# Kernel tuning notes

Measured on AMD Instinct MI355X. Metric: run time of the kernel, lower is better.

## Reference

```python
import jax, jax.numpy as jnp
import numpy as np

B, T, C, H = 4, 2048, 1024, 16
HS = C // H  # head_size = 64


def setup_inputs() -> dict:
    key = jax.random.key(0)
    ks = jax.random.split(key, 6)
    s = C ** -0.5  # Linear default init scale (approx, kaiming-uniform-ish)
    x = jax.random.normal(ks[0], (B, T, C), dtype=jnp.float32)
    Wq = jax.random.normal(ks[1], (H, C, HS), dtype=jnp.float32) * s
    Wk = jax.random.normal(ks[2], (H, C, HS), dtype=jnp.float32) * s
    Wv = jax.random.normal(ks[3], (H, C, HS), dtype=jnp.float32) * s
    Wproj = jax.random.normal(ks[4], (C, C), dtype=jnp.float32) * s
    bproj = jax.random.normal(ks[5], (C,), dtype=jnp.float32) * s
    return {"x": x, "Wq": Wq, "Wk": Wk, "Wv": Wv, "Wproj": Wproj, "bproj": bproj}


def reference(x, Wq, Wk, Wv, Wproj, bproj):
    # Batched multi-head attention equivalent to looping over per-head modules.
    # q,k,v: (B, H, T, HS)
    q = jnp.einsum('btc,hcd->bhtd', x, Wq)
    k = jnp.einsum('btc,hcd->bhtd', x, Wk)
    v = jnp.einsum('btc,hcd->bhtd', x, Wv)
    scale = HS ** -0.5
    scores = jnp.einsum('bhqd,bhkd->bhqk', q, k) * scale  # (B,H,T,T)
    causal = jnp.tril(jnp.ones((T, T), dtype=bool))
    scores = jnp.where(causal, scores, -jnp.inf)
    wei = jax.nn.softmax(scores, axis=-1)
    out_heads = jnp.einsum('bhqk,bhkd->bhqd', wei, v)  # (B,H,T,HS)
    # concat heads along last dim -> (B,T,H*HS) = (B,T,C)
    combo = out_heads.transpose(0, 2, 1, 3).reshape(B, T, C)
    out = jnp.einsum('btc,cd->btd', combo, Wproj.T.T @ jnp.eye(C, dtype=combo.dtype)) if False else combo @ Wproj.T + bproj
    # dropout p=0.0 (eval) -> identity
    return out
```

## Files before the change

kernel.cpp:

```cpp
#include <hip/hip_runtime.h>
#include <stdint.h>

#define B_  4
#define T_  2048
#define C_  1024
#define H_  16
#define HS_ 64
#define M_  (B_*T_)
#define K_  C_

typedef unsigned short u16;
typedef float v4f __attribute__((ext_vector_type(4)));
typedef short v8s __attribute__((ext_vector_type(8)));
typedef u16   v4u __attribute__((ext_vector_type(4)));
typedef unsigned int u32;
typedef u32 v2u32 __attribute__((ext_vector_type(2)));

__device__ __forceinline__ u16 f2bf(float f){
  unsigned u = __float_as_uint(f);
  u += 0x7fffu + ((u >> 16) & 1u);
  return (u16)(u >> 16);
}

__device__ __forceinline__ u32 cvt_pk_bf16(float a, float b){
  u32 r;
  asm("v_cvt_pk_bf16_f32 %0, %1, %2" : "=v"(r) : "v"(a), "v"(b));
  return r;
}

__device__ __forceinline__ void async16(const void* g, void* l){
  __builtin_amdgcn_global_load_lds(
      (const __attribute__((address_space(1))) unsigned int*)g,
      (__attribute__((address_space(3))) unsigned int*)l,
      16, 0, 0);
}


__global__ __launch_bounds__(256)
void prep(const float* __restrict__ x,
          const float* __restrict__ Wq, const float* __restrict__ Wk,
          const float* __restrict__ Wv, const float* __restrict__ Wproj,
          u16* __restrict__ xhat, u16* __restrict__ wallT, u16* __restrict__ wprojT)
{
  const int bid = blockIdx.x;
  if (bid < 4096){
    int gid = bid * 256 + threadIdx.x;
    int r  = gid >> 7;
    int kg = gid & 127;
    const float* s = x + ((size_t)r << 10) + (kg << 3);
    v4f a = *(const v4f*)s;
    v4f b = *(const v4f*)(s + 4);
    union { v8s v; u16 e[8]; } o;
    o.e[0]=f2bf(a[0]); o.e[1]=f2bf(a[1]); o.e[2]=f2bf(a[2]); o.e[3]=f2bf(a[3]);
    o.e[4]=f2bf(b[0]); o.e[5]=f2bf(b[1]); o.e[6]=f2bf(b[2]); o.e[7]=f2bf(b[3]);
    *(v8s*)(xhat + (((size_t)(r >> 4) * 128 + kg) * 128 + ((r & 15) << 3))) = o.v;
  } else if (bid < 5632){
    int gid = (bid - 4096) * 256 + threadIdx.x;
    int n  = gid >> 7;
    int cg = gid & 127;
    int tensor = n >> 10;
    int h = (n >> 6) & 15;
    int d = n & 63;
    const float* W = (tensor == 0) ? Wq : ((tensor == 1) ? Wk : Wv);
    const float* base = W + ((size_t)(h * C_ + cg * 8)) * HS_ + d;
    union { v8s v; u16 e[8]; } o;
    #pragma unroll
    for (int j = 0; j < 8; j++) o.e[j] = f2bf(base[(size_t)j * HS_]);
    *(v8s*)(wallT + (((size_t)(n >> 4) * 128 + cg) * 128 + ((n & 15) << 3))) = o.v;
  } else {
    int gid = (bid - 5632) * 256 + threadIdx.x;
    int r  = gid >> 7;
    int kg = gid & 127;
    const float* s = Wproj + ((size_t)r << 10) + (kg << 3);
    v4f a = *(const v4f*)s;
    v4f b = *(const v4f*)(s + 4);
    union { v8s v; u16 e[8]; } o;
    o.e[0]=f2bf(a[0]); o.e[1]=f2bf(a[1]); o.e[2]=f2bf(a[2]); o.e[3]=f2bf(a[3]);
    o.e[4]=f2bf(b[0]); o.e[5]=f2bf(b[1]); o.e[6]=f2bf(b[2]); o.e[7]=f2bf(b[3]);
    *(v8s*)(wprojT + (((size_t)(r >> 4) * 128 + kg) * 128 + ((r & 15) << 3))) = o.v;
  }
}

#define QSCALE 0.1803368801111204f

template<int MODE>
__global__ __launch_bounds__(256)
void gemm_bt(const u16* __restrict__ A, const u16* __restrict__ Bt,
             const float* __restrict__ bias,
             u16* __restrict__ o0, u16* __restrict__ o1, u16* __restrict__ o2,
             float* __restrict__ o0f)
{
  __shared__ __align__(16) u16 sA[2][128 * 32];
  __shared__ __align__(16) u16 sB[2][128 * 32];
  const int tid  = threadIdx.x;
  const int lane = tid & 63;
  const int wave = tid >> 6;
  const int l15  = lane & 15, quad = lane >> 4;
  const int wm   = wave >> 1, wn = wave & 1;
  const int m0   = blockIdx.y * 128;
  const int n0   = blockIdx.x * 128;
  const int mg0  = blockIdx.y * 8;
  const int ng0  = blockIdx.x * 8;

  v4f acc[4][4] = {};

  const int s0 = tid, s1 = tid + 256;
  const int t0 = s0 >> 6, r0 = s0 & 15, g0 = (s0 >> 4) & 3;
  const int t1 = s1 >> 6, r1 = s1 & 15, g1 = (s1 >> 4) & 3;

  const char* aS0 = (const char*)A  + ((size_t)(mg0 + t0) * 16384 + g0 * 128 + r0 * 8) * 2;
  const char* aS1 = (const char*)A  + ((size_t)(mg0 + t1) * 16384 + g1 * 128 + r1 * 8) * 2;
  const char* bS0 = (const char*)Bt + ((size_t)(ng0 + t0) * 16384 + g0 * 128 + r0 * 8) * 2;
  const char* bS1 = (const char*)Bt + ((size_t)(ng0 + t1) * 16384 + g1 * 128 + r1 * 8) * 2;

  async16(aS0, (char*)sA[0] + s0 * 16);
  async16(aS1, (char*)sA[0] + s1 * 16);
  async16(bS0, (char*)sB[0] + s0 * 16);
  async16(bS1, (char*)sB[0] + s1 * 16);
  __syncthreads();

  int cur = 0;
  for (int kk = 0; kk < K_; kk += 32){
    const int nxt = cur ^ 1;
    if (kk + 32 < K_){
      const size_t off = (size_t)(kk + 32) * 32;
      async16(aS0 + off, (char*)sA[nxt] + s0 * 16);
      async16(aS1 + off, (char*)sA[nxt] + s1 * 16);
      async16(bS0 + off, (char*)sB[nxt] + s0 * 16);
      async16(bS1 + off, (char*)sB[nxt] + s1 * 16);
    }

    v8s af[4], bfr[4];
    const u16* pa = sA[cur] + (size_t)(wm * 4) * 512 + lane * 8;
    const u16* pb = sB[cur] + (size_t)(wn * 4) * 512 + lane * 8;
    #pragma unroll
    for (int mi = 0; mi < 4; mi++) af[mi]  = *(const v8s*)(pa + mi * 512);
    #pragma unroll
    for (int ni = 0; ni < 4; ni++) bfr[ni] = *(const v8s*)(pb + ni * 512);

    #pragma unroll
    for (int mi = 0; mi < 4; mi++)
      #pragma unroll
      for (int ni = 0; ni < 4; ni++)
        acc[mi][ni] = __builtin_amdgcn_mfma_f32_16x16x32_bf16(af[mi], bfr[ni], acc[mi][ni], 0, 0, 0);

    __syncthreads();
    cur = nxt;
  }

  if constexpr (MODE == 0){
    #pragma unroll
    for (int ni = 0; ni < 4; ni++){
      const int ng = n0 + wn * 64 + ni * 16 + l15;
      const int tensor = ng >> 10;
      const int hh = (ng >> 6) & 15;
      const int d  = ng & 63;
      #pragma unroll
      for (int mi = 0; mi < 4; mi++){
        const int mbase = m0 + wm * 64 + mi * 16 + quad * 4;
        const int bb = mbase >> 11;
        const int tt = mbase & 2047;
        if (tensor == 2){
          v4u pk;
          #pragma unroll
          for (int r = 0; r < 4; r++) pk[r] = f2bf(acc[mi][ni][r]);
          *(v4u*)(o2 + ((size_t)((bb * H_ + hh) * HS_ + d)) * T_ + tt) = pk;
        } else if (tensor == 0){
          #pragma unroll
          for (int r = 0; r < 4; r++)
            o0[((size_t)((bb * H_ + hh)) * T_ + tt + r) * HS_ + d] = f2bf(acc[mi][ni][r] * QSCALE);
        } else {
          #pragma unroll
          for (int r = 0; r < 4; r++)
            o1[((size_t)((bb * H_ + hh)) * T_ + tt + r) * HS_ + d] = f2bf(acc[mi][ni][r]);
        }
      }
    }
  } else {
    #pragma unroll
    for (int ni = 0; ni < 4; ni++){
      const int ng = n0 + wn * 64 + ni * 16 + l15;
      const float bv = bias[ng];
      #pragma unroll
      for (int mi = 0; mi < 4; mi++){
        const int mbase = m0 + wm * 64 + mi * 16 + quad * 4;
        #pragma unroll
        for (int r = 0; r < 4; r++)
          o0f[(size_t)(mbase + r) * C_ + ng] = acc[mi][ni][r] + bv;
      }
    }
  }
}

__global__ __launch_bounds__(512, 4)
void attn(const u16* __restrict__ Q, const u16* __restrict__ Kb_, const u16* __restrict__ Vt,
          u16* __restrict__ O)
{
  __shared__ __align__(16) u16 sK[64 * 64];
  __shared__ __align__(16) u16 sV[64 * 64];
  const int tid  = threadIdx.x;
  const int lane = tid & 63;
  const int wave = tid >> 6;
  const int l15  = lane & 15, quad = lane >> 4;
  const int pp   = blockIdx.y & 7;
  const int bh   = blockIdx.x * 8 + (blockIdx.y >> 3);

  const u16* Qb = Q   + (size_t)bh * T_ * HS_;
  const u16* Kb = Kb_ + (size_t)bh * T_ * HS_;
  const u16* Vb = Vt  + (size_t)bh * HS_ * T_;
  const int b = bh >> 4, h = bh & 15;

  const int g  = tid;
  const int tg = g >> 3;
  const int sw = ((g & 7) ^ (tg & 7)) << 4;
  const char* Kby = (const char*)Kb;
  const char* Vby = (const char*)Vb;
  const int koff = tg * 128 + sw;
  const int voff = tg * (T_ * 2) + sw;
  char* sKp = (char*)sK + g * 16;
  char* sVp = (char*)sV + g * 16;

  const int fsw0 = (quad ^ (l15 & 7)) * 8;
  const int fsw1 = ((quad + 4) ^ (l15 & 7)) * 8;

  #pragma unroll 1
  for (int ph = 0; ph < 2; ph++){
    const int qt = ph ? (15 - pp) : pp;
    const int q0 = qt * 128 + wave * 16;

    const v8s qf0 = *(const v8s*)(Qb + (size_t)(q0 + l15) * HS_ + quad * 8);
    const v8s qf1 = *(const v8s*)(Qb + (size_t)(q0 + l15) * HS_ + 32 + quad * 8);

    v4f Oa[4] = {};
    float lsum = 0.f;

    const int ktmax = 2 * qt + 1;
    for (int kt = 0; kt <= ktmax; kt++){
      const int k0 = kt * 64;
      async16(Kby + (size_t)k0 * 128 + koff, sKp);
      async16(Vby + (size_t)k0 * 2   + voff, sVp);
      __syncthreads();

      if (k0 <= q0 + 15){
        v4f sacc[4] = {};
        __builtin_amdgcn_s_setprio(1);
        #pragma unroll
        for (int nt = 0; nt < 4; nt++){
          const u16* kr = sK + (nt * 16 + l15) * 64;
          v8s kf0 = *(const v8s*)(kr + fsw0);
          v8s kf1 = *(const v8s*)(kr + fsw1);
          sacc[nt] = __builtin_amdgcn_mfma_f32_16x16x32_bf16(kf0, qf0, sacc[nt], 0, 0, 0);
          sacc[nt] = __builtin_amdgcn_mfma_f32_16x16x32_bf16(kf1, qf1, sacc[nt], 0, 0, 0);
        }
        __builtin_amdgcn_s_setprio(0);
        const bool diag = (k0 + 63 > q0);
        const int qrow_rel = (q0 - k0) + l15;

        u32 pw[4][2];
        #pragma unroll
        for (int nt = 0; nt < 4; nt++){
          float p0 = exp2f(sacc[nt][0]);
          float p1 = exp2f(sacc[nt][1]);
          float p2 = exp2f(sacc[nt][2]);
          float p3 = exp2f(sacc[nt][3]);
          if (diag){
            const int kbase = nt * 16 + quad * 4;
            if (kbase + 0 > qrow_rel) p0 = 0.f;
            if (kbase + 1 > qrow_rel) p1 = 0.f;
            if (kbase + 2 > qrow_rel) p2 = 0.f;
            if (kbase + 3 > qrow_rel) p3 = 0.f;
          }
          lsum += (p0 + p1) + (p2 + p3);
          pw[nt][0] = cvt_pk_bf16(p0, p1);
          pw[nt][1] = cvt_pk_bf16(p2, p3);
        }

        u32 a0 = pw[0][0], c0 = pw[1][0];
        asm("v_permlane32_swap_b32 %0, %1" : "+v"(a0), "+v"(c0));
        asm("v_permlane16_swap_b32 %0, %1" : "+v"(a0), "+v"(c0));
        u32 a1 = pw[0][1], c1 = pw[1][1];
        asm("v_permlane32_swap_b32 %0, %1" : "+v"(a1), "+v"(c1));
        asm("v_permlane16_swap_b32 %0, %1" : "+v"(a1), "+v"(c1));
        u32 b0 = pw[2][0], d0 = pw[3][0];
        asm("v_permlane32_swap_b32 %0, %1" : "+v"(b0), "+v"(d0));
        asm("v_permlane16_swap_b32 %0, %1" : "+v"(b0), "+v"(d0));
        u32 b1 = pw[2][1], d1 = pw[3][1];
        asm("v_permlane32_swap_b32 %0, %1" : "+v"(b1), "+v"(d1));
        asm("v_permlane16_swap_b32 %0, %1" : "+v"(b1), "+v"(d1));
        union { u32 u[4]; v8s v; } P0, P1;
        P0.u[0] = a0; P0.u[1] = a1; P0.u[2] = c0; P0.u[3] = c1;
        P1.u[0] = b0; P1.u[1] = b1; P1.u[2] = d0; P1.u[3] = d1;

        __builtin_amdgcn_s_setprio(1);
        #pragma unroll
        for (int nt = 0; nt < 4; nt++){
          const u16* vr = sV + (nt * 16 + l15) * 64;
          v8s vf0 = *(const v8s*)(vr + fsw0);
          v8s vf1 = *(const v8s*)(vr + fsw1);
          Oa[nt] = __builtin_amdgcn_mfma_f32_16x16x32_bf16(P0.v, vf0, Oa[nt], 0, 0, 0);
          Oa[nt] = __builtin_amdgcn_mfma_f32_16x16x32_bf16(P1.v, vf1, Oa[nt], 0, 0, 0);
        }
        __builtin_amdgcn_s_setprio(0);
      }
      __syncthreads();
    }

    float rs = lsum;
    rs += __shfl_xor(rs, 16);
    rs += __shfl_xor(rs, 32);
    const int mg = b * 128 + qt * 8 + wave;
    #pragma unroll
    for (int reg = 0; reg < 4; reg++){
      const float rsq = __shfl(rs, quad * 4 + reg);
      const float inv = (rsq > 0.f) ? (1.f / rsq) : 0.f;
      const int mrow = quad * 4 + reg;
      #pragma unroll
      for (int nt = 0; nt < 4; nt++){
        const int cg = h * 8 + nt * 2 + (l15 >> 3);
        O[((size_t)mg * 128 + cg) * 128 + mrow * 8 + (l15 & 7)] = f2bf(Oa[nt][reg] * inv);
      }
    }
  }
}

extern "C" void kernel_launch(void* const* d_in, const int* in_sizes, int n_in,
                              void* d_out, int out_size, void* d_ws, size_t ws_size,
                              hipStream_t stream)
{
  const float* x     = (const float*)d_in[0];
  const float* Wq    = (const float*)d_in[1];
  const float* Wk    = (const float*)d_in[2];
  const float* Wv    = (const float*)d_in[3];
  const float* Wproj = (const float*)d_in[4];
  const float* bproj = (const float*)d_in[5];
  float* out = (float*)d_out;

  u16* xhat   = (u16*)d_ws;
  u16* att    = xhat;
  u16* q_ws   = xhat  + (size_t)M_ * C_;
  u16* k_ws   = q_ws  + (size_t)M_ * C_;
  u16* vt_ws  = k_ws  + (size_t)M_ * C_;
  u16* wallT  = vt_ws + (size_t)M_ * C_;
  u16* wprojT = wallT + (size_t)3 * C_ * K_;

  prep<<<dim3(6144), dim3(256), 0, stream>>>(x, Wq, Wk, Wv, Wproj, xhat, wallT, wprojT);
  gemm_bt<0><<<dim3(24, 64), dim3(256), 0, stream>>>(xhat, wallT, nullptr,
                                                     q_ws, k_ws, vt_ws, nullptr);
  attn<<<dim3(8, 64), dim3(512), 0, stream>>>(q_ws, k_ws, vt_ws, att);
  gemm_bt<1><<<dim3(8, 64), dim3(256), 0, stream>>>(att, wprojT, bproj,
                                                    nullptr, nullptr, nullptr, out);
}
```

Baseline: 278.6 us.

## Shrink attention query tile to 64 rows with 4-wave blocks

The attention kernel now uses 256-thread blocks that each own a 64-row query tile, with twice as many blocks along the grid's y dimension. Each thread issues two async 16-byte copies per K and V tile instead of one, and global pointers are advanced incrementally. Because the query tile now matches the key tile height, every wave runs every iteration, so the per-wave skip branch for fully masked key tiles is removed. The aim is to cut idle waves on causal-diagonal tiles and to improve load balance and occupancy, at the cost of loading each K/V tile into shared memory more times overall.

```diff
diff --git a/kernel.cpp b/kernel.cpp
--- a/kernel.cpp
+++ b/kernel.cpp
@@ -192,7 +192,7 @@
   }
 }
 
-__global__ __launch_bounds__(512, 4)
+__global__ __launch_bounds__(256, 4)
 void attn(const u16* __restrict__ Q, const u16* __restrict__ Kb_, const u16* __restrict__ Vt,
           u16* __restrict__ O)
 {
@@ -202,31 +202,30 @@
   const int lane = tid & 63;
   const int wave = tid >> 6;
   const int l15  = lane & 15, quad = lane >> 4;
-  const int pp   = blockIdx.y & 7;
-  const int bh   = blockIdx.x * 8 + (blockIdx.y >> 3);
+  const int pp   = blockIdx.y & 15;
+  const int bh   = blockIdx.x * 8 + (blockIdx.y >> 4);
 
   const u16* Qb = Q   + (size_t)bh * T_ * HS_;
   const u16* Kb = Kb_ + (size_t)bh * T_ * HS_;
   const u16* Vb = Vt  + (size_t)bh * HS_ * T_;
   const int b = bh >> 4, h = bh & 15;
 
-  const int g  = tid;
-  const int tg = g >> 3;
-  const int sw = ((g & 7) ^ (tg & 7)) << 4;
-  const char* Kby = (const char*)Kb;
-  const char* Vby = (const char*)Vb;
-  const int koff = tg * 128 + sw;
-  const int voff = tg * (T_ * 2) + sw;
-  char* sKp = (char*)sK + g * 16;
-  char* sVp = (char*)sV + g * 16;
+  const int g0 = tid, g1 = tid + 256;
+  const int t0g = g0 >> 3, t1g = g1 >> 3;
+  const int sw0 = ((g0 & 7) ^ (t0g & 7)) << 4;
+  const int sw1 = ((g1 & 7) ^ (t1g & 7)) << 4;
+  const int koff0 = t0g * 128 + sw0,        koff1 = t1g * 128 + sw1;
+  const int voff0 = t0g * (T_ * 2) + sw0,   voff1 = t1g * (T_ * 2) + sw1;
+  char* sKp0 = (char*)sK + g0 * 16;  char* sKp1 = (char*)sK + g1 * 16;
+  char* sVp0 = (char*)sV + g0 * 16;  char* sVp1 = (char*)sV + g1 * 16;
 
   const int fsw0 = (quad ^ (l15 & 7)) * 8;
   const int fsw1 = ((quad + 4) ^ (l15 & 7)) * 8;
 
   #pragma unroll 1
   for (int ph = 0; ph < 2; ph++){
-    const int qt = ph ? (15 - pp) : pp;
-    const int q0 = qt * 128 + wave * 16;
+    const int qt = ph ? (31 - pp) : pp;
+    const int q0 = qt * 64 + wave * 16;
 
     const v8s qf0 = *(const v8s*)(Qb + (size_t)(q0 + l15) * HS_ + quad * 8);
     const v8s qf1 = *(const v8s*)(Qb + (size_t)(q0 + l15) * HS_ + 32 + quad * 8);
@@ -234,81 +233,83 @@
     v4f Oa[4] = {};
     float lsum = 0.f;
 
-    const int ktmax = 2 * qt + 1;
-    for (int kt = 0; kt <= ktmax; kt++){
+    const char* kp0 = (const char*)Kb + koff0;  const char* kp1 = (const char*)Kb + koff1;
+    const char* vp0 = (const char*)Vb + voff0;  const char* vp1 = (const char*)Vb + voff1;
+
+    for (int kt = 0; kt <= qt; kt++){
       const int k0 = kt * 64;
-      async16(Kby + (size_t)k0 * 128 + koff, sKp);
-      async16(Vby + (size_t)k0 * 2   + voff, sVp);
+      async16(kp0, sKp0);  async16(kp1, sKp1);
+      async16(vp0, sVp0);  async16(vp1, sVp1);
+      kp0 += 64 * 128; kp1 += 64 * 128;
+      vp0 += 128;      vp1 += 128;
       __syncthreads();
 
-      if (k0 <= q0 + 15){
-        v4f sacc[4] = {};
-        __builtin_amdgcn_s_setprio(1);
-        #pragma unroll
-        for (int nt = 0; nt < 4; nt++){
-          const u16* kr = sK + (nt * 16 + l15) * 64;
-          v8s kf0 = *(const v8s*)(kr + fsw0);
-          v8s kf1 = *(const v8s*)(kr + fsw1);
-          sacc[nt] = __builtin_amdgcn_mfma_f32_16x16x32_bf16(kf0, qf0, sacc[nt], 0, 0, 0);
-          sacc[nt] = __builtin_amdgcn_mfma_f32_16x16x32_bf16(kf1, qf1, sacc[nt], 0, 0, 0);
+      v4f sacc[4] = {};
+      __builtin_amdgcn_s_setprio(1);
+      #pragma unroll
+      for (int nt = 0; nt < 4; nt++){
+        const u16* kr = sK + (nt * 16 + l15) * 64;
+        v8s kf0 = *(const v8s*)(kr + fsw0);
+        v8s kf1 = *(const v8s*)(kr + fsw1);
+        sacc[nt] = __builtin_amdgcn_mfma_f32_16x16x32_bf16(kf0, qf0, sacc[nt], 0, 0, 0);
+        sacc[nt] = __builtin_amdgcn_mfma_f32_16x16x32_bf16(kf1, qf1, sacc[nt], 0, 0, 0);
+      }
+      __builtin_amdgcn_s_setprio(0);
+      const bool diag = (k0 + 63 > q0);
+      const int qrow_rel = (q0 - k0) + l15;
+
+      u32 pw[4][2];
+      #pragma unroll
+      for (int nt = 0; nt < 4; nt++){
+        float p0 = exp2f(sacc[nt][0]);
+        float p1 = exp2f(sacc[nt][1]);
+        float p2 = exp2f(sacc[nt][2]);
+        float p3 = exp2f(sacc[nt][3]);
+        if (diag){
+          const int kbase = nt * 16 + quad * 4;
+          if (kbase + 0 > qrow_rel) p0 = 0.f;
+          if (kbase + 1 > qrow_rel) p1 = 0.f;
+          if (kbase + 2 > qrow_rel) p2 = 0.f;
+          if (kbase + 3 > qrow_rel) p3 = 0.f;
         }
-        __builtin_amdgcn_s_setprio(0);
-        const bool diag = (k0 + 63 > q0);
-        const int qrow_rel = (q0 - k0) + l15;
-
-        u32 pw[4][2];
-        #pragma unroll
-        for (int nt = 0; nt < 4; nt++){
-          float p0 = exp2f(sacc[nt][0]);
-          float p1 = exp2f(sacc[nt][1]);
-          float p2 = exp2f(sacc[nt][2]);
-          float p3 = exp2f(sacc[nt][3]);
-          if (diag){
-            const int kbase = nt * 16 + quad * 4;
-            if (kbase + 0 > qrow_rel) p0 = 0.f;
-            if (kbase + 1 > qrow_rel) p1 = 0.f;
-            if (kbase + 2 > qrow_rel) p2 = 0.f;
-            if (kbase + 3 > qrow_rel) p3 = 0.f;
-          }
-          lsum += (p0 + p1) + (p2 + p3);
-          pw[nt][0] = cvt_pk_bf16(p0, p1);
-          pw[nt][1] = cvt_pk_bf16(p2, p3);
-        }
-
-        u32 a0 = pw[0][0], c0 = pw[1][0];
-        asm("v_permlane32_swap_b32 %0, %1" : "+v"(a0), "+v"(c0));
-        asm("v_permlane16_swap_b32 %0, %1" : "+v"(a0), "+v"(c0));
-        u32 a1 = pw[0][1], c1 = pw[1][1];
-        asm("v_permlane32_swap_b32 %0, %1" : "+v"(a1), "+v"(c1));
-        asm("v_permlane16_swap_b32 %0, %1" : "+v"(a1), "+v"(c1));
-        u32 b0 = pw[2][0], d0 = pw[3][0];
-        asm("v_permlane32_swap_b32 %0, %1" : "+v"(b0), "+v"(d0));
-        asm("v_permlane16_swap_b32 %0, %1" : "+v"(b0), "+v"(d0));
-        u32 b1 = pw[2][1], d1 = pw[3][1];
-        asm("v_permlane32_swap_b32 %0, %1" : "+v"(b1), "+v"(d1));
-        asm("v_permlane16_swap_b32 %0, %1" : "+v"(b1), "+v"(d1));
-        union { u32 u[4]; v8s v; } P0, P1;
-        P0.u[0] = a0; P0.u[1] = a1; P0.u[2] = c0; P0.u[3] = c1;
-        P1.u[0] = b0; P1.u[1] = b1; P1.u[2] = d0; P1.u[3] = d1;
-
-        __builtin_amdgcn_s_setprio(1);
-        #pragma unroll
-        for (int nt = 0; nt < 4; nt++){
-          const u16* vr = sV + (nt * 16 + l15) * 64;
-          v8s vf0 = *(const v8s*)(vr + fsw0);
-          v8s vf1 = *(const v8s*)(vr + fsw1);
-          Oa[nt] = __builtin_amdgcn_mfma_f32_16x16x32_bf16(P0.v, vf0, Oa[nt], 0, 0, 0);
-          Oa[nt] = __builtin_amdgcn_mfma_f32_16x16x32_bf16(P1.v, vf1, Oa[nt], 0, 0, 0);
-        }
-        __builtin_amdgcn_s_setprio(0);
-      }
+        lsum += (p0 + p1) + (p2 + p3);
+        pw[nt][0] = cvt_pk_bf16(p0, p1);
+        pw[nt][1] = cvt_pk_bf16(p2, p3);
+      }
+
+      u32 a0 = pw[0][0], c0 = pw[1][0];
+      asm("v_permlane32_swap_b32 %0, %1" : "+v"(a0), "+v"(c0));
+      asm("v_permlane16_swap_b32 %0, %1" : "+v"(a0), "+v"(c0));
+      u32 a1 = pw[0][1], c1 = pw[1][1];
+      asm("v_permlane32_swap_b32 %0, %1" : "+v"(a1), "+v"(c1));
+      asm("v_permlane16_swap_b32 %0, %1" : "+v"(a1), "+v"(c1));
+      u32 b0 = pw[2][0], d0 = pw[3][0];
+      asm("v_permlane32_swap_b32 %0, %1" : "+v"(b0), "+v"(d0));
+      asm("v_permlane16_swap_b32 %0, %1" : "+v"(b0), "+v"(d0));
+      u32 b1 = pw[2][1], d1 = pw[3][1];
+      asm("v_permlane32_swap_b32 %0, %1" : "+v"(b1), "+v"(d1));
+      asm("v_permlane16_swap_b32 %0, %1" : "+v"(b1), "+v"(d1));
+      union { u32 u[4]; v8s v; } P0, P1;
+      P0.u[0] = a0; P0.u[1] = a1; P0.u[2] = c0; P0.u[3] = c1;
+      P1.u[0] = b0; P1.u[1] = b1; P1.u[2] = d0; P1.u[3] = d1;
+
+      __builtin_amdgcn_s_setprio(1);
+      #pragma unroll
+      for (int nt = 0; nt < 4; nt++){
+        const u16* vr = sV + (nt * 16 + l15) * 64;
+        v8s vf0 = *(const v8s*)(vr + fsw0);
+        v8s vf1 = *(const v8s*)(vr + fsw1);
+        Oa[nt] = __builtin_amdgcn_mfma_f32_16x16x32_bf16(P0.v, vf0, Oa[nt], 0, 0, 0);
+        Oa[nt] = __builtin_amdgcn_mfma_f32_16x16x32_bf16(P1.v, vf1, Oa[nt], 0, 0, 0);
+      }
+      __builtin_amdgcn_s_setprio(0);
       __syncthreads();
     }
 
     float rs = lsum;
     rs += __shfl_xor(rs, 16);
     rs += __shfl_xor(rs, 32);
-    const int mg = b * 128 + qt * 8 + wave;
+    const int mg = b * 128 + qt * 4 + wave;
     #pragma unroll
     for (int reg = 0; reg < 4; reg++){
       const float rsq = __shfl(rs, quad * 4 + reg);
@@ -346,7 +347,7 @@
   prep<<<dim3(6144), dim3(256), 0, stream>>>(x, Wq, Wk, Wv, Wproj, xhat, wallT, wprojT);
   gemm_bt<0><<<dim3(24, 64), dim3(256), 0, stream>>>(xhat, wallT, nullptr,
                                                      q_ws, k_ws, vt_ws, nullptr);
-  attn<<<dim3(8, 64), dim3(512), 0, stream>>>(q_ws, k_ws, vt_ws, att);
+  attn<<<dim3(8, 128), dim3(256), 0, stream>>>(q_ws, k_ws, vt_ws, att);
   gemm_bt<1><<<dim3(8, 64), dim3(256), 0, stream>>>(att, wprojT, bproj,
                                                     nullptr, nullptr, nullptr, out);
 }
```

After: 280.0 us. Within noise of the previous version (+0.5%).
